# Kernel tuning notes

Hardware: AMD Instinct MI355X
Metric: run time of the kernel (lower is better)

The kernel has to match this reference:

```python
import jax, jax.numpy as jnp
import numpy as np

N_HEAD = 16
P_MIN, P_MAX = 1e-4, 1e3
V_MIN = 1e-10
SHIFT = 5.0


def setup_inputs() -> dict:
    key = jax.random.key(0)
    ks = jax.random.split(key, 4)
    B, T, C = 2, 2048, 1024
    x = jax.random.normal(ks[0], (B, T, C), dtype=jnp.float32)
    w_attn = jax.random.normal(ks[1], (C, 3 * C), dtype=jnp.float32) * 0.02
    b_attn = jnp.zeros((3 * C,), dtype=jnp.float32)
    w_proj = jax.random.normal(ks[2], (C, C), dtype=jnp.float32) * 0.02
    b_proj = jnp.zeros((C,), dtype=jnp.float32)
    p_param = jnp.ones((C,), dtype=jnp.float32)
    return {"x": x, "w_attn": w_attn, "b_attn": b_attn,
            "w_proj": w_proj, "b_proj": b_proj, "p_param": p_param}


def reference(x, w_attn, b_attn, w_proj, b_proj, p_param):
    B, T, C = x.shape
    H = N_HEAD
    d = C // H

    qkv = x @ w_attn + b_attn                      # [B,T,3C]
    q, k, v = jnp.split(qkv, 3, axis=2)

    # signed, clamped power exponent per channel: (sign(p)+0.5).sign() * clamp(|p|)
    p = jnp.sign(jnp.sign(p_param) + 0.5) * jnp.clip(jnp.abs(p_param), P_MIN, P_MAX)

    # log-power transform of V with max-subtraction over T for stability
    v = jnp.clip(jnp.abs(v + SHIFT), V_MIN, None)  # [B,T,C]
    z = p * jnp.log(v)
    z_max = jnp.max(z, axis=1, keepdims=True)      # [B,1,C]
    v = jnp.exp(z - z_max)

    # heads: [B,H,T,d]
    q = q.reshape(B, T, H, d).transpose(0, 2, 1, 3)
    k = k.reshape(B, T, H, d).transpose(0, 2, 1, 3)
    v = v.reshape(B, T, H, d).transpose(0, 2, 1, 3)

    scale = 1.0 / jnp.sqrt(jnp.float32(d))
    scores = jnp.einsum('bhqd,bhkd->bhqk', q, k) * scale
    causal = jnp.tril(jnp.ones((T, T), dtype=bool))
    scores = jnp.where(causal, scores, -jnp.inf)
    att = jax.nn.softmax(scores, axis=-1)
    mean = jnp.einsum('bhqk,bhkd->bhqd', att, v)   # [B,H,T,d]
    mean = mean.transpose(0, 2, 1, 3).reshape(B, T, C)

    # invert the log-power transform (generalized power mean)
    y = jnp.exp((z_max + jnp.log(mean)) / p) - SHIFT
    return y @ w_proj + b_proj
```

## Files before the change

### kernel.cpp

```cpp
#include <hip/hip_runtime.h>
#include <hip/hip_bf16.h>
#include <math.h>

constexpr int B_ = 2;
constexpr int T_ = 2048;
constexpr int C_ = 1024;
constexpr int H_ = 16;
constexpr int D_ = 64;
constexpr int M_ = B_ * T_;
constexpr float SHIFT_ = 5.0f;
constexpr float P_MIN_ = 1e-4f;
constexpr float P_MAX_ = 1e3f;
constexpr float V_MIN_ = 1e-10f;
typedef __attribute__((ext_vector_type(8))) short s16x8;
typedef __attribute__((ext_vector_type(4))) short s16x4;
typedef __attribute__((ext_vector_type(8))) _Float16 h16x8;
typedef __attribute__((ext_vector_type(4))) float f32x4;
typedef unsigned short ushort_t;

__device__ __forceinline__ float clamp_p(float pp) {
    float s = (pp >= 0.f) ? 1.f : -1.f;
    return s * fminf(fmaxf(fabsf(pp), P_MIN_), P_MAX_);
}

__device__ __forceinline__ ushort_t f2h(float f) {
    _Float16 h = (_Float16)f;
    return __builtin_bit_cast(unsigned short, h);
}
__device__ __forceinline__ float h2f(ushort_t h) {
    return (float)__builtin_bit_cast(_Float16, h);
}

__device__ __forceinline__ float fast_exp2(float x) {
#if __has_builtin(__builtin_amdgcn_exp2f)
    return __builtin_amdgcn_exp2f(x);
#else
    return __expf(x * 0.6931471805599453f);
#endif
}

__device__ __forceinline__ void gload_lds16(const void* g, void* l) {
    __builtin_amdgcn_global_load_lds(
        (const __attribute__((address_space(1))) unsigned int*)g,
        (__attribute__((address_space(3))) unsigned int*)l, 16, 0, 0);
}

__global__ __launch_bounds__(256)
void conv_h(const float* __restrict__ src, ushort_t* __restrict__ hi) {
    int idx = blockIdx.x * 256 + threadIdx.x;
    float4 f = ((const float4*)src)[idx];
    ushort4 h;
    h.x = f2h(f.x); h.y = f2h(f.y); h.z = f2h(f.z); h.w = f2h(f.w);
    ((ushort4*)hi)[idx] = h;
}

__global__ __launch_bounds__(256)
void convT_h(const float* __restrict__ W, ushort_t* __restrict__ Wth,
             int N, int K) {
    __shared__ float tile[64][65];
    const int k0 = blockIdx.y * 64, n0 = blockIdx.x * 64;
    const int tr = threadIdx.x >> 4;
    const int tc4 = (threadIdx.x & 15) * 4;
#pragma unroll
    for (int i = 0; i < 4; ++i) {
        float4 f = *(const float4*)&W[(size_t)(k0 + tr + i * 16) * N + n0 + tc4];
        tile[tr + i * 16][tc4 + 0] = f.x;
        tile[tr + i * 16][tc4 + 1] = f.y;
        tile[tr + i * 16][tc4 + 2] = f.z;
        tile[tr + i * 16][tc4 + 3] = f.w;
    }
    __syncthreads();
#pragma unroll
    for (int i = 0; i < 4; ++i) {
        int n = tr + i * 16;
        ushort4 h;
        h.x = f2h(tile[tc4 + 0][n]);
        h.y = f2h(tile[tc4 + 1][n]);
        h.z = f2h(tile[tc4 + 2][n]);
        h.w = f2h(tile[tc4 + 3][n]);
        *(ushort4*)&Wth[(size_t)(n0 + n) * K + k0 + tc4] = h;
    }
}

__global__ __launch_bounds__(256)
void gemm1(const ushort_t* __restrict__ Ah, const ushort_t* __restrict__ Bh,
           const float* __restrict__ bias, float* __restrict__ Cm,
           int M, int N, int K) {
    __shared__ ushort_t Lds[2 * 2 * 128 * 32];

    const int tid = threadIdx.x;
    const int w = tid >> 6;
    const int lane = tid & 63;
    const int l16 = lane & 15;
    const int quad = lane >> 4;
    const int row0 = blockIdx.y * 128, col0 = blockIdx.x * 128;
    const int wr = w >> 1, wc = w & 1;

    const ushort_t* gb[8];
    ushort_t* lb[8];
#pragma unroll
    for (int j = 0; j < 8; ++j) {
        int q = j * 4 + w;
        int plane = q >> 4;
        int cc = q & 15;
        int sub = cc & 1;
        int r = (cc >> 1) * 16 + (lane >> 2);
        const ushort_t* src = plane ? Bh : Ah;
        int tb = plane ? col0 : row0;
        gb[j] = src + (size_t)(tb + r) * K + sub * 32 + (lane & 3) * 8;
        lb[j] = &Lds[plane * 8192 + sub * 4096 + r * 32 + (lane & 3) * 8];
    }

    f32x4 acc[4][4] = {};

    for (int k0 = 0; k0 < K; k0 += 64) {
        __syncthreads();
#pragma unroll
        for (int j = 0; j < 8; ++j)
            gload_lds16(gb[j] + k0, lb[j]);
        __syncthreads();

#pragma unroll
        for (int kk = 0; kk < 2; ++kk) {
            h16x8 af[4], bf[4];
#pragma unroll
            for (int mi = 0; mi < 4; ++mi)
                af[mi] = *(const h16x8*)&Lds[kk * 4096 + (wr * 64 + mi * 16 + l16) * 32 + quad * 8];
#pragma unroll
            for (int ni = 0; ni < 4; ++ni)
                bf[ni] = *(const h16x8*)&Lds[8192 + kk * 4096 + (wc * 64 + ni * 16 + l16) * 32 + quad * 8];
#pragma unroll
            for (int mi = 0; mi < 4; ++mi)
#pragma unroll
                for (int ni = 0; ni < 4; ++ni)
                    acc[mi][ni] = __builtin_amdgcn_mfma_f32_16x16x32_f16(af[mi], bf[ni], acc[mi][ni], 0, 0, 0);
        }
    }

#pragma unroll
    for (int mi = 0; mi < 4; ++mi) {
#pragma unroll
        for (int r = 0; r < 4; ++r) {
            int row = row0 + wr * 64 + mi * 16 + quad * 4 + r;
#pragma unroll
            for (int ni = 0; ni < 4; ++ni) {
                int col = col0 + wc * 64 + ni * 16 + l16;
                Cm[(size_t)row * N + col] = acc[mi][ni][r] + bias[col];
            }
        }
    }
}

__global__ __launch_bounds__(256)
void zmax_part(const float* __restrict__ qkv, const float* __restrict__ p_param,
               float* __restrict__ zpart) {
    const int tch = blockIdx.x & 15;
    const int ctile = (blockIdx.x >> 4) & 15;
    const int b = blockIdx.x >> 8;
    const int col = threadIdx.x & 63;
    const int r = threadIdx.x >> 6;
    const int c = ctile * 64 + col;

    const float p = clamp_p(p_param[c]);
    const float* vp = qkv + (size_t)b * T_ * 3 * C_
                    + (size_t)(tch * 128) * 3 * C_ + 2 * C_ + c;

    float lm = -INFINITY;
    for (int t = r; t < 128; t += 4) {
        float v = vp[(size_t)t * 3 * C_];
        float z = p * __logf(fmaxf(fabsf(v + SHIFT_), V_MIN_));
        lm = fmaxf(lm, z);
    }
    __shared__ float red[4][64];
    red[r][col] = lm;
    __syncthreads();
    if (threadIdx.x < 64) {
        float m = fmaxf(fmaxf(red[0][threadIdx.x], red[1][threadIdx.x]),
                        fmaxf(red[2][threadIdx.x], red[3][threadIdx.x]));
        zpart[((size_t)b * 16 + tch) * C_ + ctile * 64 + threadIdx.x] = m;
    }
}

__global__ __launch_bounds__(256)
void zmax_fin(const float* __restrict__ zpart, float* __restrict__ zmax) {
    int idx = blockIdx.x * 256 + threadIdx.x;
    int b = idx >> 10;
    int c = idx & (C_ - 1);
    float m = -INFINITY;
#pragma unroll
    for (int ch = 0; ch < 16; ++ch)
        m = fmaxf(m, zpart[((size_t)b * 16 + ch) * C_ + c]);
    zmax[idx] = m;
}

__global__ __launch_bounds__(256)
void prep_kv(const float* __restrict__ qkv, const float* __restrict__ p_param,
             const float* __restrict__ zmax,
             ushort_t* __restrict__ kbf, ushort_t* __restrict__ vtbf) {
    __shared__ ushort_t VtL[64 * 72];

    const int blk = blockIdx.x;
    const int tt = blk & 31;
    const int bh = blk >> 5;
    const int b = bh >> 4;
    const int h = bh & 15;
    const int t0 = tt * 64;

    const int tl = threadIdx.x >> 2;
    const int c0 = (threadIdx.x & 3) * 16;
    const int g0 = c0 >> 3;
    const int ptl = (tl & 15) * 4 + (tl >> 4);

    const size_t rowbase = (size_t)b * T_ * 3 * C_ + (size_t)(t0 + tl) * 3 * C_ + h * D_;

    {
        const float* ksrc = qkv + rowbase + C_ + c0;
        ushort_t tk[16];
#pragma unroll
        for (int u = 0; u < 16; u += 4) {
            float4 f = *(const float4*)&ksrc[u];
            tk[u + 0] = f2h(f.x); tk[u + 1] = f2h(f.y);
            tk[u + 2] = f2h(f.z); tk[u + 3] = f2h(f.w);
        }
        size_t krow = ((size_t)bh * T_ + t0 + tl) * 64;
        *(s16x8*)&kbf[krow + ((g0)     ^ (tl & 7)) * 8] = *(s16x8*)&tk[0];
        *(s16x8*)&kbf[krow + ((g0 + 1) ^ (tl & 7)) * 8] = *(s16x8*)&tk[8];
    }

    {
        const float* vsrc = qkv + rowbase + 2 * C_ + c0;
#pragma unroll
        for (int u = 0; u < 16; u += 4) {
            float4 f = *(const float4*)&vsrc[u];
            float vv[4] = {f.x, f.y, f.z, f.w};
#pragma unroll
            for (int q = 0; q < 4; ++q) {
                int c = h * D_ + c0 + u + q;
                float p = clamp_p(p_param[c]);
                float z = p * __logf(fmaxf(fabsf(vv[q] + SHIFT_), V_MIN_));
                float val = __expf(z - zmax[b * C_ + c]);
                VtL[(c0 + u + q) * 72 + ptl] = f2h(val);
            }
        }
    }
    __syncthreads();
    {
        const int d = tl;
        s16x8 r0 = *(const s16x8*)&VtL[d * 72 + c0];
        s16x8 r1 = *(const s16x8*)&VtL[d * 72 + c0 + 8];
        size_t vbase = ((size_t)bh * 32 + tt) * 4096 + (size_t)d * 64;
        *(s16x8*)&vtbf[vbase + ((g0)     ^ (d & 7)) * 8] = r0;
        *(s16x8*)&vtbf[vbase + ((g0 + 1) ^ (d & 7)) * 8] = r1;
    }
}

__device__ __forceinline__ void load_kfrag(h16x8 kf[2][4], const ushort_t* tile,
                                           int l16, int sg0, int sg1) {
#pragma unroll
    for (int nt = 0; nt < 4; ++nt) {
        kf[0][nt] = *(const h16x8*)&tile[(nt * 16 + l16) * 64 + sg0];
        kf[1][nt] = *(const h16x8*)&tile[(nt * 16 + l16) * 64 + sg1];
    }
}

__device__ __forceinline__ void tile_body2(const h16x8 qf[2][2], const h16x8 kf[2][4],
        const h16x8 vf[2][4], const h16x8 ones, bool diag, int l16, int quad, int qh,
        ushort_t* psw, f32x4 O[2][4], f32x4 Ol[2]) {
#pragma unroll
    for (int m = 0; m < 2; ++m) {
        f32x4 s[4] = {};
#pragma unroll
        for (int nt = 0; nt < 4; ++nt) {
            s[nt] = __builtin_amdgcn_mfma_f32_16x16x32_f16(qf[m][0], kf[0][nt], s[nt], 0, 0, 0);
            s[nt] = __builtin_amdgcn_mfma_f32_16x16x32_f16(qf[m][1], kf[1][nt], s[nt], 0, 0, 0);
        }

        if (diag) {
#pragma unroll
            for (int nt = 0; nt < 4; ++nt) {
                int col = nt * 16 + l16;
#pragma unroll
                for (int r = 0; r < 4; ++r) {
                    int row = qh * 32 + m * 16 + quad * 4 + r;
                    if (col > row) s[nt][r] = -3.0e38f;
                }
            }
        }

#pragma unroll
        for (int r = 0; r < 4; ++r) {
            ushort_t t4[4];
#pragma unroll
            for (int nt = 0; nt < 4; ++nt)
                t4[nt] = f2h(fast_exp2(s[nt][r]));
            *(s16x4*)&psw[(quad * 4 + r) * 72 + l16 * 4] = *(const s16x4*)t4;
        }

#pragma unroll
        for (int ks = 0; ks < 2; ++ks) {
            h16x8 afr = *(const h16x8*)&psw[l16 * 72 + ks * 32 + quad * 8];
            Ol[m] = __builtin_amdgcn_mfma_f32_16x16x32_f16(afr, ones, Ol[m], 0, 0, 0);
#pragma unroll
            for (int nt = 0; nt < 4; ++nt)
                O[m][nt] = __builtin_amdgcn_mfma_f32_16x16x32_f16(afr, vf[ks][nt], O[m][nt], 0, 0, 0);
        }
    }
}

__global__ __launch_bounds__(256, 2)
void attn_mfma(float* qkv,
               const ushort_t* __restrict__ kbf, const ushort_t* __restrict__ vtbf,
               float* __restrict__ ml) {
    __shared__ ushort_t Ps[4][16 * 72];
    __shared__ float Osum[2][32][65];
    __shared__ float Lsum[2][32];

    const int tid = threadIdx.x;
    const int w = tid >> 6;
    const int lane = tid & 63;
    const int l16 = lane & 15;
    const int quad = lane >> 4;
    const int qh = w >> 1;
    const int kp = w & 1;

    const int qt = 31 - (blockIdx.x >> 5);
    const int bh = blockIdx.x & 31;
    const int b = bh >> 4;
    const int h = bh & 15;
    const int q0 = qt * 64;

    const int sg0 = ((0 + quad) ^ (l16 & 7)) * 8;
    const int sg1 = ((4 + quad) ^ (l16 & 7)) * 8;

    f32x4 O[2][4] = {};
    f32x4 Ol[2] = {};

    h16x8 ones;
#pragma unroll
    for (int i = 0; i < 8; ++i) ones[i] = (_Float16)1.0f;

    h16x8 qf[2][2];
#pragma unroll
    for (int m = 0; m < 2; ++m) {
        const int qrow = q0 + qh * 32 + m * 16 + l16;
        const float* qrp = qkv + (size_t)b * T_ * 3 * C_
                         + (size_t)qrow * 3 * C_ + h * D_;
#pragma unroll
        for (int ks = 0; ks < 2; ++ks) {
            const float QS = 0.125f * 1.4426950408889634f;
            float4 f0 = *(const float4*)&qrp[ks * 32 + quad * 8];
            float4 f1 = *(const float4*)&qrp[ks * 32 + quad * 8 + 4];
            ushort_t t8[8];
            t8[0] = f2h(f0.x * QS); t8[1] = f2h(f0.y * QS);
            t8[2] = f2h(f0.z * QS); t8[3] = f2h(f0.w * QS);
            t8[4] = f2h(f1.x * QS); t8[5] = f2h(f1.y * QS);
            t8[6] = f2h(f1.z * QS); t8[7] = f2h(f1.w * QS);
            qf[m][ks] = *(h16x8*)t8;
        }
    }

    const ushort_t* khead = kbf + (size_t)bh * T_ * 64;
    const ushort_t* vhead = vtbf + (size_t)bh * 32 * 4096;
    ushort_t* psw = &Ps[w][0];

    if (kp <= qt) {
        h16x8 kfA[2][4], kfB[2][4], vfA[2][4], vfB[2][4];
        load_kfrag(kfA, khead + (size_t)kp * 4096, l16, sg0, sg1);
        load_kfrag(vfA, vhead + (size_t)kp * 4096, l16, sg0, sg1);

        for (int kt = kp; kt <= qt; kt += 4) {
            int ktB = (kt + 2 <= qt) ? kt + 2 : kt;
            load_kfrag(kfB, khead + (size_t)ktB * 4096, l16, sg0, sg1);
            load_kfrag(vfB, vhead + (size_t)ktB * 4096, l16, sg0, sg1);
            tile_body2(qf, kfA, vfA, ones, kt == qt, l16, quad, qh, psw, O, Ol);
            if (kt + 2 > qt) break;
            int ktA = (kt + 4 <= qt) ? kt + 4 : kt + 2;
            load_kfrag(kfA, khead + (size_t)ktA * 4096, l16, sg0, sg1);
            load_kfrag(vfA, vhead + (size_t)ktA * 4096, l16, sg0, sg1);
            tile_body2(qf, kfB, vfB, ones, kt + 2 == qt, l16, quad, qh, psw, O, Ol);
        }
    }

    if (kp == 0) {
#pragma unroll
        for (int m = 0; m < 2; ++m)
#pragma unroll
            for (int r = 0; r < 4; ++r) {
                int lr = m * 16 + quad * 4 + r;
#pragma unroll
                for (int nt = 0; nt < 4; ++nt)
                    Osum[qh][lr][nt * 16 + l16] = O[m][nt][r];
                if (l16 == 0) Lsum[qh][lr] = Ol[m][r];
            }
    }
    __syncthreads();
    if (kp == 1) {
#pragma unroll
        for (int m = 0; m < 2; ++m)
#pragma unroll
            for (int r = 0; r < 4; ++r) {
                int lr = m * 16 + quad * 4 + r;
                int t = q0 + qh * 32 + lr;
                float* dst = qkv + (size_t)(b * T_ + t) * 3 * C_ + C_ + h * D_;
#pragma unroll
                for (int nt = 0; nt < 4; ++nt)
                    dst[nt * 16 + l16] = O[m][nt][r] + Osum[qh][lr][nt * 16 + l16];
                if (l16 == 0)
                    ml[bh * T_ + t] = Ol[m][r] + Lsum[qh][lr];
            }
    }
}

__global__ __launch_bounds__(256)
void combine_y(const float* __restrict__ qkv, const float* __restrict__ p_param,
               const float* __restrict__ zmax, const float* __restrict__ ml,
               ushort_t* __restrict__ yh) {
    int idx = blockIdx.x * 256 + threadIdx.x;
    int n4 = idx * 4;
    int c = n4 & (C_ - 1);
    int bt = n4 >> 10;
    int t = bt & (T_ - 1);
    int b = bt >> 11;
    int h = c >> 6;
    int bh = b * H_ + h;

    float inv_den = 1.f / ml[bh * T_ + t];

    const float* base = qkv + (size_t)bt * 3 * C_;
    float4 O0 = *(const float4*)&base[C_ + c];
    float4 zm = *(const float4*)&zmax[b * C_ + c];
    float4 pp = *(const float4*)&p_param[c];

    ushort4 hh;
    {
        float mean = O0.x * inv_den;
        float y = expf((zm.x + logf(mean)) / clamp_p(pp.x)) - SHIFT_;
        hh.x = f2h(y);
    }
    {
        float mean = O0.y * inv_den;
        float y = expf((zm.y + logf(mean)) / clamp_p(pp.y)) - SHIFT_;
        hh.y = f2h(y);
    }
    {
        float mean = O0.z * inv_den;
        float y = expf((zm.z + logf(mean)) / clamp_p(pp.z)) - SHIFT_;
        hh.z = f2h(y);
    }
    {
        float mean = O0.w * inv_den;
        float y = expf((zm.w + logf(mean)) / clamp_p(pp.w)) - SHIFT_;
        hh.w = f2h(y);
    }
    ((ushort4*)yh)[idx] = hh;
}

extern "C" void kernel_launch(void* const* d_in, const int* in_sizes, int n_in,
                              void* d_out, int out_size, void* d_ws, size_t ws_size,
                              hipStream_t stream) {
    const float* x      = (const float*)d_in[0];
    const float* w_attn = (const float*)d_in[1];
    const float* b_attn = (const float*)d_in[2];
    const float* w_proj = (const float*)d_in[3];
    const float* b_proj = (const float*)d_in[4];
    const float* p_par  = (const float*)d_in[5];
    float* out = (float*)d_out;

    char* ws = (char*)d_ws;
    float* qkv = (float*)ws;
    char* p1 = ws + (size_t)M_ * 3 * C_ * sizeof(float);
    ushort_t* xh = (ushort_t*)p1;
    ushort_t* xl = xh + (size_t)M_ * C_;
    ushort_t* wth = xl + (size_t)M_ * C_;
    ushort_t* wtl = wth + (size_t)3 * C_ * C_;
    float* zmax = (float*)(wtl + (size_t)3 * C_ * C_);
    ushort_t* kbf  = (ushort_t*)((char*)zmax + B_ * C_ * sizeof(float));
    ushort_t* vtbf = kbf + (size_t)B_ * H_ * T_ * 64;
    float* ml = (float*)(vtbf + (size_t)B_ * H_ * T_ * 64);
    float* zpart = ml + 2 * 32 * T_;

    conv_h<<<M_ * C_ / 1024, 256, 0, stream>>>(x, xh);
    convT_h<<<dim3(3 * C_ / 64, C_ / 64), 256, 0, stream>>>(w_attn, wth, 3 * C_, C_);
    gemm1<<<dim3(3 * C_ / 128, M_ / 128), 256, 0, stream>>>(xh, wth,
                                                            b_attn, qkv, M_, 3 * C_, C_);
    zmax_part<<<B_ * 16 * 16, 256, 0, stream>>>(qkv, p_par, zpart);
    zmax_fin<<<B_ * C_ / 256, 256, 0, stream>>>(zpart, zmax);
    prep_kv<<<B_ * H_ * 32, 256, 0, stream>>>(qkv, p_par, zmax, kbf, vtbf);
    attn_mfma<<<B_ * H_ * (T_ / 64), 256, 0, stream>>>(qkv, kbf, vtbf, ml);
    combine_y<<<M_ * C_ / 1024, 256, 0, stream>>>(qkv, p_par, zmax, ml, xh);
    convT_h<<<dim3(C_ / 64, C_ / 64), 256, 0, stream>>>(w_proj, wth, C_, C_);
    gemm1<<<dim3(C_ / 128, M_ / 128), 256, 0, stream>>>(xh, wth,
                                                        b_proj, out, M_, C_, C_);
}
```

Measured before the change: 216.6 us.

## Keep attention probabilities in registers by transposing the score MFMA

Swaps the operand order of the QK^T MFMA so each lane's score fragment already matches the A-operand layout of the PV MFMA. The exponentiated probabilities are packed directly into registers instead of going through an LDS round trip, which removes the per-wave shared buffer. The V^T key ordering in prep_kv is permuted to match the new fragment layout, and the causal mask indexing is updated to fit. Separately, the finalize kernel switches to the fast __expf/__logf intrinsics, trading some accuracy for cheaper transcendentals.

```diff
diff --git a/kernel.cpp b/kernel.cpp
--- a/kernel.cpp
+++ b/kernel.cpp
@@ -209,7 +209,8 @@
     const int tl = threadIdx.x >> 2;
     const int c0 = (threadIdx.x & 3) * 16;
     const int g0 = c0 >> 3;
-    const int ptl = (tl & 15) * 4 + (tl >> 4);
+    const int ptl = ((tl >> 5) & 1) * 32 + ((tl >> 2) & 3) * 8
+                  + ((tl >> 4) & 1) * 4 + (tl & 3);
 
     const size_t rowbase = (size_t)b * T_ * 3 * C_ + (size_t)(t0 + tl) * 3 * C_ + h * D_;
 
@@ -265,44 +266,40 @@
 
 __device__ __forceinline__ void tile_body2(const h16x8 qf[2][2], const h16x8 kf[2][4],
         const h16x8 vf[2][4], const h16x8 ones, bool diag, int l16, int quad, int qh,
-        ushort_t* psw, f32x4 O[2][4], f32x4 Ol[2]) {
+        f32x4 O[2][4], f32x4 Ol[2]) {
 #pragma unroll
     for (int m = 0; m < 2; ++m) {
         f32x4 s[4] = {};
 #pragma unroll
         for (int nt = 0; nt < 4; ++nt) {
-            s[nt] = __builtin_amdgcn_mfma_f32_16x16x32_f16(qf[m][0], kf[0][nt], s[nt], 0, 0, 0);
-            s[nt] = __builtin_amdgcn_mfma_f32_16x16x32_f16(qf[m][1], kf[1][nt], s[nt], 0, 0, 0);
+            s[nt] = __builtin_amdgcn_mfma_f32_16x16x32_f16(kf[0][nt], qf[m][0], s[nt], 0, 0, 0);
+            s[nt] = __builtin_amdgcn_mfma_f32_16x16x32_f16(kf[1][nt], qf[m][1], s[nt], 0, 0, 0);
         }
 
         if (diag) {
-#pragma unroll
-            for (int nt = 0; nt < 4; ++nt) {
-                int col = nt * 16 + l16;
+            int row = qh * 32 + m * 16 + l16;
+#pragma unroll
+            for (int nt = 0; nt < 4; ++nt)
 #pragma unroll
                 for (int r = 0; r < 4; ++r) {
-                    int row = qh * 32 + m * 16 + quad * 4 + r;
+                    int col = nt * 16 + quad * 4 + r;
                     if (col > row) s[nt][r] = -3.0e38f;
                 }
+        }
+
+#pragma unroll
+        for (int ks = 0; ks < 2; ++ks) {
+            ushort_t t8[8];
+#pragma unroll
+            for (int r = 0; r < 4; ++r) {
+                t8[r]     = f2h(fast_exp2(s[2 * ks][r]));
+                t8[4 + r] = f2h(fast_exp2(s[2 * ks + 1][r]));
             }
-        }
-
-#pragma unroll
-        for (int r = 0; r < 4; ++r) {
-            ushort_t t4[4];
+            h16x8 pa = *(const h16x8*)t8;
+            Ol[m] = __builtin_amdgcn_mfma_f32_16x16x32_f16(pa, ones, Ol[m], 0, 0, 0);
 #pragma unroll
             for (int nt = 0; nt < 4; ++nt)
-                t4[nt] = f2h(fast_exp2(s[nt][r]));
-            *(s16x4*)&psw[(quad * 4 + r) * 72 + l16 * 4] = *(const s16x4*)t4;
-        }
-
-#pragma unroll
-        for (int ks = 0; ks < 2; ++ks) {
-            h16x8 afr = *(const h16x8*)&psw[l16 * 72 + ks * 32 + quad * 8];
-            Ol[m] = __builtin_amdgcn_mfma_f32_16x16x32_f16(afr, ones, Ol[m], 0, 0, 0);
-#pragma unroll
-            for (int nt = 0; nt < 4; ++nt)
-                O[m][nt] = __builtin_amdgcn_mfma_f32_16x16x32_f16(afr, vf[ks][nt], O[m][nt], 0, 0, 0);
+                O[m][nt] = __builtin_amdgcn_mfma_f32_16x16x32_f16(pa, vf[ks][nt], O[m][nt], 0, 0, 0);
         }
     }
 }
@@ -311,7 +308,6 @@
 void attn_mfma(float* qkv,
                const ushort_t* __restrict__ kbf, const ushort_t* __restrict__ vtbf,
                float* __restrict__ ml) {
-    __shared__ ushort_t Ps[4][16 * 72];
     __shared__ float Osum[2][32][65];
     __shared__ float Lsum[2][32];
 
@@ -361,7 +357,6 @@
 
     const ushort_t* khead = kbf + (size_t)bh * T_ * 64;
     const ushort_t* vhead = vtbf + (size_t)bh * 32 * 4096;
-    ushort_t* psw = &Ps[w][0];
 
     if (kp <= qt) {
         h16x8 kfA[2][4], kfB[2][4], vfA[2][4], vfB[2][4];
@@ -372,12 +367,12 @@
             int ktB = (kt + 2 <= qt) ? kt + 2 : kt;
             load_kfrag(kfB, khead + (size_t)ktB * 4096, l16, sg0, sg1);
             load_kfrag(vfB, vhead + (size_t)ktB * 4096, l16, sg0, sg1);
-            tile_body2(qf, kfA, vfA, ones, kt == qt, l16, quad, qh, psw, O, Ol);
+            tile_body2(qf, kfA, vfA, ones, kt == qt, l16, quad, qh, O, Ol);
             if (kt + 2 > qt) break;
             int ktA = (kt + 4 <= qt) ? kt + 4 : kt + 2;
             load_kfrag(kfA, khead + (size_t)ktA * 4096, l16, sg0, sg1);
             load_kfrag(vfA, vhead + (size_t)ktA * 4096, l16, sg0, sg1);
-            tile_body2(qf, kfB, vfB, ones, kt + 2 == qt, l16, quad, qh, psw, O, Ol);
+            tile_body2(qf, kfB, vfB, ones, kt + 2 == qt, l16, quad, qh, O, Ol);
         }
     }
 
@@ -434,22 +429,22 @@
     ushort4 hh;
     {
         float mean = O0.x * inv_den;
-        float y = expf((zm.x + logf(mean)) / clamp_p(pp.x)) - SHIFT_;
+        float y = __expf((zm.x + __logf(mean)) / clamp_p(pp.x)) - SHIFT_;
         hh.x = f2h(y);
     }
     {
         float mean = O0.y * inv_den;
-        float y = expf((zm.y + logf(mean)) / clamp_p(pp.y)) - SHIFT_;
+        float y = __expf((zm.y + __logf(mean)) / clamp_p(pp.y)) - SHIFT_;
         hh.y = f2h(y);
     }
     {
         float mean = O0.z * inv_den;
-        float y = expf((zm.z + logf(mean)) / clamp_p(pp.z)) - SHIFT_;
+        float y = __expf((zm.z + __logf(mean)) / clamp_p(pp.z)) - SHIFT_;
         hh.z = f2h(y);
     }
     {
         float mean = O0.w * inv_den;
-        float y = expf((zm.w + logf(mean)) / clamp_p(pp.w)) - SHIFT_;
+        float y = __expf((zm.w + __logf(mean)) / clamp_p(pp.w)) - SHIFT_;
         hh.w = f2h(y);
     }
     ((ushort4*)yh)[idx] = hh;
```

New measurement: 215.7 us. About the same (-0.4%).
